# Performance work log

Measured on AMD Instinct MI355X. Metric: run time of the kernel, lower is better.

The kernel has to match this reference:

```python
import jax, jax.numpy as jnp
import numpy as np


def setup_inputs() -> dict:
    key = jax.random.key(0)
    k1, k2 = jax.random.split(key)
    y = jax.random.normal(k1, (2048, 256), dtype=jnp.float32)  # (num_labels, 2*hidden)
    x = jax.random.normal(k2, (1024, 128), dtype=jnp.float32)  # (batch, hidden)
    return {"y": y, "x": x}


def reference(y, x):
    h = y.shape[-1] // 2
    # box parameters: min coordinate and softplus delta
    mn = y[:, :h][None, :, :]                      # (1, L, h)
    delta = jax.nn.softplus(y[:, h:])[None, :, :]  # (1, L, h)
    mx = mn + delta
    center = mn + delta / 2.0
    dp1 = delta + 1.0
    xr = x[:, None, :]                             # (B, 1, h)
    l1 = jnp.abs(xr - center)                      # (B, L, h)
    inside = (mn <= xr) & (xr <= mx)
    outside_dist = l1 * dp1 - delta / 2.0 * (delta - 1.0 / (delta + 1e-10))
    per_dim = jnp.where(inside, l1 / (dp1 + 1e-10), outside_dist)
    distance = jnp.linalg.norm(per_dim, axis=-1)   # (B, L)
    return -distance
```

## Files before the change

kernel.cpp:

```cpp
#include <hip/hip_runtime.h>
#include <hip/hip_bf16.h>
#include <math.h>


#define BM 32
#define BN 64
#define TM 8

__global__ __launch_bounds__(256) void boxe_prep(const float* __restrict__ y,
                                                 float4* __restrict__ p4)
{
    __shared__ float t0[128][9], t1[128][9], t2[128][9], t3[128][9];
    const int tid = threadIdx.x;
    const int n0  = blockIdx.x * 8;

#pragma unroll
    for (int i = 0; i < 4; ++i) {
        int j  = i * 256 + tid;
        int k  = j & 127;
        int nl = j >> 7;
        int n  = n0 + nl;
        float mn = y[n * 256 + k];
        float dv = y[n * 256 + 128 + k];
        float delta = fmaxf(dv, 0.0f) + log1pf(expf(-fabsf(dv)));
        float hd  = 0.5f * delta;
        t0[k][nl] = mn + hd;
        t1[k][nl] = hd;
        t2[k][nl] = 1.0f / (delta + 1.0f + 1e-10f);
        t3[k][nl] = hd * (delta - 1.0f / (delta + 1e-10f));
    }
    __syncthreads();

#pragma unroll
    for (int i = 0; i < 4; ++i) {
        int j  = i * 256 + tid;
        int nl = j & 7;
        int k  = j >> 3;
        p4[k * 2048 + n0 + nl] =
            make_float4(t0[k][nl], t1[k][nl], t2[k][nl], t3[k][nl]);
    }
}

__global__ __launch_bounds__(256, 4) void boxe_main(
    const float4* __restrict__ p4, const float* __restrict__ x,
    float* __restrict__ out)
{
    const int tid  = threadIdx.x;
    const int lane = tid & 63;
    const int wave = __builtin_amdgcn_readfirstlane(tid >> 6);
    const int m0   = blockIdx.y * BM + wave * TM;
    const int n    = blockIdx.x * BN + lane;

    const float* xr0 = x + (m0 + 0) * 128;
    const float* xr1 = x + (m0 + 1) * 128;
    const float* xr2 = x + (m0 + 2) * 128;
    const float* xr3 = x + (m0 + 3) * 128;
    const float* xr4 = x + (m0 + 4) * 128;
    const float* xr5 = x + (m0 + 5) * 128;
    const float* xr6 = x + (m0 + 6) * 128;
    const float* xr7 = x + (m0 + 7) * 128;

    const float4* pp = p4 + n;

    float acc0 = 0.0f, acc1 = 0.0f, acc2 = 0.0f, acc3 = 0.0f;
    float acc4 = 0.0f, acc5 = 0.0f, acc6 = 0.0f, acc7 = 0.0f;

#define EVAL(ACC, XS)                                                     \
    do {                                                                  \
        float l = fabsf((XS) - p.x);                                      \
        float v = (l <= p.y) ? (l * p.z) : fmaf(l, dp1, -p.w);            \
        ACC = fmaf(v, v, ACC);                                            \
    } while (0)

#pragma unroll 8
    for (int k = 0; k < 128; ++k) {
        float4 p  = pp[k * 2048];
        float dp1 = fmaf(2.0f, p.y, 1.0f);
        EVAL(acc0, xr0[k]);
        EVAL(acc1, xr1[k]);
        EVAL(acc2, xr2[k]);
        EVAL(acc3, xr3[k]);
        EVAL(acc4, xr4[k]);
        EVAL(acc5, xr5[k]);
        EVAL(acc6, xr6[k]);
        EVAL(acc7, xr7[k]);
    }
#undef EVAL

    out[(m0 + 0) * 2048 + n] = -sqrtf(acc0);
    out[(m0 + 1) * 2048 + n] = -sqrtf(acc1);
    out[(m0 + 2) * 2048 + n] = -sqrtf(acc2);
    out[(m0 + 3) * 2048 + n] = -sqrtf(acc3);
    out[(m0 + 4) * 2048 + n] = -sqrtf(acc4);
    out[(m0 + 5) * 2048 + n] = -sqrtf(acc5);
    out[(m0 + 6) * 2048 + n] = -sqrtf(acc6);
    out[(m0 + 7) * 2048 + n] = -sqrtf(acc7);
}

extern "C" void kernel_launch(void* const* d_in, const int* in_sizes, int n_in,
                              void* d_out, int out_size, void* d_ws, size_t ws_size,
                              hipStream_t stream) {
    const float* y = (const float*)d_in[0];
    const float* x = (const float*)d_in[1];
    float* out = (float*)d_out;

    float4* p4 = (float4*)d_ws;

    hipLaunchKernelGGL(boxe_prep, dim3(2048 / 8), dim3(256), 0, stream, y, p4);

    dim3 grid(2048 / BN, 1024 / BM);
    hipLaunchKernelGGL(boxe_main, grid, dim3(256), 0, stream, p4, x, out);
}
```

Measured before the change: 115.8 us.

## Preload x rows into registers, broadcast via readlane, double-buffer box params

Each wave now loads its 8 x rows once into VGPRs (two halves per lane) and broadcasts each element with readlane, replacing per-iteration scalar/global loads of x. Box parameter float4 loads are software-pipelined into two register banks of 8 so the next loads are in flight while the current ones are evaluated. This is meant to hide global load latency and cut load instruction count, at the cost of more VGPRs, which may lower occupancy under launch_bounds(256,4).

```diff
diff --git a/kernel.cpp b/kernel.cpp
--- a/kernel.cpp
+++ b/kernel.cpp
@@ -51,41 +51,108 @@
     const int m0   = blockIdx.y * BM + wave * TM;
     const int n    = blockIdx.x * BN + lane;
 
-    const float* xr0 = x + (m0 + 0) * 128;
-    const float* xr1 = x + (m0 + 1) * 128;
-    const float* xr2 = x + (m0 + 2) * 128;
-    const float* xr3 = x + (m0 + 3) * 128;
-    const float* xr4 = x + (m0 + 4) * 128;
-    const float* xr5 = x + (m0 + 5) * 128;
-    const float* xr6 = x + (m0 + 6) * 128;
-    const float* xr7 = x + (m0 + 7) * 128;
+    const float* xb = x + m0 * 128 + lane;
+    float xA0 = xb[0 * 128];      float xB0 = xb[0 * 128 + 64];
+    float xA1 = xb[1 * 128];      float xB1 = xb[1 * 128 + 64];
+    float xA2 = xb[2 * 128];      float xB2 = xb[2 * 128 + 64];
+    float xA3 = xb[3 * 128];      float xB3 = xb[3 * 128 + 64];
+    float xA4 = xb[4 * 128];      float xB4 = xb[4 * 128 + 64];
+    float xA5 = xb[5 * 128];      float xB5 = xb[5 * 128 + 64];
+    float xA6 = xb[6 * 128];      float xB6 = xb[6 * 128 + 64];
+    float xA7 = xb[7 * 128];      float xB7 = xb[7 * 128 + 64];
 
     const float4* pp = p4 + n;
 
     float acc0 = 0.0f, acc1 = 0.0f, acc2 = 0.0f, acc3 = 0.0f;
     float acc4 = 0.0f, acc5 = 0.0f, acc6 = 0.0f, acc7 = 0.0f;
 
-#define EVAL(ACC, XS)                                                     \
-    do {                                                                  \
-        float l = fabsf((XS) - p.x);                                      \
-        float v = (l <= p.y) ? (l * p.z) : fmaf(l, dp1, -p.w);            \
-        ACC = fmaf(v, v, ACC);                                            \
+#define RL(V, LI) __int_as_float(__builtin_amdgcn_readlane(__float_as_int(V), (LI)))
+
+#define EVAL(ACC, SX, P, DP1)                                              \
+    do {                                                                   \
+        float l = fabsf((SX) - (P).x);                                     \
+        float v = (l <= (P).y) ? (l * (P).z) : fmaf(l, (DP1), -(P).w);     \
+        ACC = fmaf(v, v, ACC);                                             \
     } while (0)
 
-#pragma unroll 8
-    for (int k = 0; k < 128; ++k) {
-        float4 p  = pp[k * 2048];
-        float dp1 = fmaf(2.0f, p.y, 1.0f);
-        EVAL(acc0, xr0[k]);
-        EVAL(acc1, xr1[k]);
-        EVAL(acc2, xr2[k]);
-        EVAL(acc3, xr3[k]);
-        EVAL(acc4, xr4[k]);
-        EVAL(acc5, xr5[k]);
-        EVAL(acc6, xr6[k]);
-        EVAL(acc7, xr7[k]);
+#define STEPX(P, KK, H)                                                    \
+    do {                                                                   \
+        int li = (KK) & 63;                                                \
+        float sx0 = RL(x##H##0, li);                                       \
+        float sx1 = RL(x##H##1, li);                                       \
+        float sx2 = RL(x##H##2, li);                                       \
+        float sx3 = RL(x##H##3, li);                                       \
+        float sx4 = RL(x##H##4, li);                                       \
+        float sx5 = RL(x##H##5, li);                                       \
+        float sx6 = RL(x##H##6, li);                                       \
+        float sx7 = RL(x##H##7, li);                                       \
+        float dp1 = fmaf(2.0f, (P).y, 1.0f);           \
+        EVAL(acc0, sx0, P, dp1);                                           \
+        EVAL(acc1, sx1, P, dp1);                                           \
+        EVAL(acc2, sx2, P, dp1);                                           \
+        EVAL(acc3, sx3, P, dp1);                                           \
+        EVAL(acc4, sx4, P, dp1);                                           \
+        EVAL(acc5, sx5, P, dp1);                                           \
+        EVAL(acc6, sx6, P, dp1);                                           \
+        EVAL(acc7, sx7, P, dp1);                                           \
+    } while (0)
+
+#define LOADR(R0) do {                                                     \
+        r0 = pp[((R0) + 0) * 2048]; r1 = pp[((R0) + 1) * 2048];            \
+        r2 = pp[((R0) + 2) * 2048]; r3 = pp[((R0) + 3) * 2048];            \
+        r4 = pp[((R0) + 4) * 2048]; r5 = pp[((R0) + 5) * 2048];            \
+        r6 = pp[((R0) + 6) * 2048]; r7 = pp[((R0) + 7) * 2048];            \
+    } while (0)
+
+#define LOADQ(R0) do {                                                     \
+        q0 = pp[((R0) + 0) * 2048]; q1 = pp[((R0) + 1) * 2048];            \
+        q2 = pp[((R0) + 2) * 2048]; q3 = pp[((R0) + 3) * 2048];            \
+        q4 = pp[((R0) + 4) * 2048]; q5 = pp[((R0) + 5) * 2048];            \
+        q6 = pp[((R0) + 6) * 2048]; q7 = pp[((R0) + 7) * 2048];            \
+    } while (0)
+
+    float4 q0 = pp[0 * 2048], q1 = pp[1 * 2048], q2 = pp[2 * 2048],
+           q3 = pp[3 * 2048], q4 = pp[4 * 2048], q5 = pp[5 * 2048],
+           q6 = pp[6 * 2048], q7 = pp[7 * 2048];
+    float4 r0, r1, r2, r3, r4, r5, r6, r7;
+
+    for (int kb = 0; kb < 64; kb += 16) {
+        LOADR(kb + 8);
+        STEPX(q0, kb + 0, A); STEPX(q1, kb + 1, A);
+        STEPX(q2, kb + 2, A); STEPX(q3, kb + 3, A);
+        STEPX(q4, kb + 4, A); STEPX(q5, kb + 5, A);
+        STEPX(q6, kb + 6, A); STEPX(q7, kb + 7, A);
+        LOADQ(kb + 16);
+        STEPX(r0, kb + 8, A);  STEPX(r1, kb + 9, A);
+        STEPX(r2, kb + 10, A); STEPX(r3, kb + 11, A);
+        STEPX(r4, kb + 12, A); STEPX(r5, kb + 13, A);
+        STEPX(r6, kb + 14, A); STEPX(r7, kb + 15, A);
     }
+    for (int kb = 64; kb < 112; kb += 16) {
+        LOADR(kb + 8);
+        STEPX(q0, kb + 0, B); STEPX(q1, kb + 1, B);
+        STEPX(q2, kb + 2, B); STEPX(q3, kb + 3, B);
+        STEPX(q4, kb + 4, B); STEPX(q5, kb + 5, B);
+        STEPX(q6, kb + 6, B); STEPX(q7, kb + 7, B);
+        LOADQ(kb + 16);
+        STEPX(r0, kb + 8, B);  STEPX(r1, kb + 9, B);
+        STEPX(r2, kb + 10, B); STEPX(r3, kb + 11, B);
+        STEPX(r4, kb + 12, B); STEPX(r5, kb + 13, B);
+        STEPX(r6, kb + 14, B); STEPX(r7, kb + 15, B);
+    }
+    LOADR(120);
+    STEPX(q0, 112, B); STEPX(q1, 113, B); STEPX(q2, 114, B);
+    STEPX(q3, 115, B); STEPX(q4, 116, B); STEPX(q5, 117, B);
+    STEPX(q6, 118, B); STEPX(q7, 119, B);
+    STEPX(r0, 120, B); STEPX(r1, 121, B); STEPX(r2, 122, B);
+    STEPX(r3, 123, B); STEPX(r4, 124, B); STEPX(r5, 125, B);
+    STEPX(r6, 126, B); STEPX(r7, 127, B);
+
+#undef STEPX
 #undef EVAL
+#undef RL
+#undef LOADR
+#undef LOADQ
 
     out[(m0 + 0) * 2048 + n] = -sqrtf(acc0);
     out[(m0 + 1) * 2048 + n] = -sqrtf(acc1);
```

Result: slower. 177.3 us (+53.1%).
